# Optimization experiments

Measured on AMD Instinct MI355X. Metric: run time of the kernel, lower is better.

Reference implementation:

```python
import jax, jax.numpy as jnp
import numpy as np

NG = 100000   # num gene nodes
ND = 100000   # num disease nodes
E = 400000    # edges per edge type
EL = 200000   # label edges
C = 128       # hidden_channels


def segment_softmax(logits, seg, n):
    # PyG-style softmax over segments (numerically stable, eps=1e-16)
    m = jax.ops.segment_max(logits, seg, num_segments=n)
    e = jnp.exp(logits - m[seg])
    s = jax.ops.segment_sum(e, seg, num_segments=n)
    return e / (s[seg] + 1e-16)


def hgat_edge_type(x_src, x_dst, src_idx, dst_idx, edge_emb, wi, wj, we, att_b, n_dst):
    # gather (message), per-edge attention logit = [x_i|x_j|e] @ w  (split to avoid concat)
    x_i = x_dst[dst_idx]                                   # [E, C]
    x_j = x_src[src_idx]                                   # [E, C]
    logit = x_i @ wi + x_j @ wj + edge_emb @ we + att_b    # [E, 1] (num_heads=1)
    alpha = jax.nn.leaky_relu(logit, 0.2)
    alpha = segment_softmax(alpha, dst_idx, n_dst)
    out = jax.ops.segment_sum(x_i * alpha, dst_idx, num_segments=n_dst)  # scatter-add
    return jax.nn.relu(out)


def setup_inputs() -> dict:
    key = jax.random.key(0)
    ks = jax.random.split(key, 24)
    s = 0.02
    return {
        "x_gene": jax.random.normal(ks[0], (NG, C), jnp.float32),
        "x_disease": jax.random.normal(ks[1], (ND, C), jnp.float32),
        "edge_index_g2d": jnp.stack([jax.random.randint(ks[2], (E,), 0, NG),
                                     jax.random.randint(ks[3], (E,), 0, ND)]),
        "edge_index_d2g": jnp.stack([jax.random.randint(ks[4], (E,), 0, ND),
                                     jax.random.randint(ks[5], (E,), 0, NG)]),
        "edge_emb_g2d": jax.random.normal(ks[6], (E, C), jnp.float32),
        "edge_emb_d2g": jax.random.normal(ks[7], (E, C), jnp.float32),
        "edge_label_index": jnp.stack([jax.random.randint(ks[8], (EL,), 0, NG),
                                       jax.random.randint(ks[9], (EL,), 0, ND)]),
        # HeteroDictLinear node / edge weights (stored [in, out])
        "Wn_gene": jax.random.normal(ks[10], (C, C), jnp.float32) * s,
        "bn_gene": jnp.zeros((C,), jnp.float32),
        "Wn_disease": jax.random.normal(ks[11], (C, C), jnp.float32) * s,
        "bn_disease": jnp.zeros((C,), jnp.float32),
        "We_g2d": jax.random.normal(ks[12], (C, C), jnp.float32) * s,
        "be_g2d": jnp.zeros((C,), jnp.float32),
        "We_d2g": jax.random.normal(ks[13], (C, C), jnp.float32) * s,
        "be_d2g": jnp.zeros((C,), jnp.float32),
        # attention head: Linear(3*C, 1) applied to cat([x_i, x_j, edge_emb])
        "att_w": jax.random.normal(ks[14], (3 * C, 1), jnp.float32) * s,
        "att_b": jnp.zeros((1,), jnp.float32),
        # decoder
        "W1": jax.random.normal(ks[15], (2 * C, C), jnp.float32) * s,
        "b1": jnp.zeros((C,), jnp.float32),
        "W2": jax.random.normal(ks[16], (C, 1), jnp.float32) * s,
        "b2": jnp.zeros((1,), jnp.float32),
    }


def reference(x_gene, x_disease, edge_index_g2d, edge_index_d2g, edge_emb_g2d,
              edge_emb_d2g, edge_label_index, Wn_gene, bn_gene, Wn_disease,
              bn_disease, We_g2d, be_g2d, We_d2g, be_d2g, att_w, att_b,
              W1, b1, W2, b2):
    # per-type node / edge linear projections
    x_g = x_gene @ Wn_gene + bn_gene
    x_d = x_disease @ Wn_disease + bn_disease
    e_g2d = edge_emb_g2d @ We_g2d + be_g2d
    e_d2g = edge_emb_d2g @ We_d2g + be_d2g
    wi, wj, we = att_w[:C], att_w[C:2 * C], att_w[2 * C:]
    # gene->disease aggregates into disease nodes; disease->gene into gene nodes
    z_disease = hgat_edge_type(x_g, x_d, edge_index_g2d[0], edge_index_g2d[1],
                               e_g2d, wi, wj, we, att_b, ND)
    z_gene = hgat_edge_type(x_d, x_g, edge_index_d2g[0], edge_index_d2g[1],
                            e_d2g, wi, wj, we, att_b, NG)
    # decoder on label edges
    row, col = edge_label_index[0], edge_label_index[1]
    z = jnp.concatenate([z_gene[row], z_disease[col]], axis=-1)  # [EL, 2C]
    h = jax.nn.relu(z @ W1 + b1)
    pred = (h @ W2 + b2).reshape(-1)                             # [EL]
    return pred, z_gene, z_disease
```

## Files before the change

### kernel.cpp

```cpp
#include <hip/hip_runtime.h>
#include <hip/hip_bf16.h>
#include <stdint.h>

#define NGn 100000
#define NDn 100000
#define NEn 400000
#define ELn 200000

typedef __bf16 bf16x8 __attribute__((ext_vector_type(8)));
typedef float  f32x4  __attribute__((ext_vector_type(4)));

__device__ __forceinline__ bf16x8 cvt8(const float* __restrict__ f) {
    f32x4 a = *(const f32x4*)f;
    f32x4 b = *(const f32x4*)(f + 4);
    bf16x8 r;
    r[0] = (__bf16)a[0]; r[1] = (__bf16)a[1]; r[2] = (__bf16)a[2]; r[3] = (__bf16)a[3];
    r[4] = (__bf16)b[0]; r[5] = (__bf16)b[1]; r[6] = (__bf16)b[2]; r[7] = (__bf16)b[3];
    return r;
}

__global__ void scatter_mask(const int* __restrict__ g2d_dst,
                             const int* __restrict__ d2g_dst,
                             uint8_t* __restrict__ mask_d,
                             uint8_t* __restrict__ mask_g, int n) {
    int i = blockIdx.x * blockDim.x + threadIdx.x;
    if (i < n) {
        mask_d[g2d_dst[i]] = 1;
        mask_g[d2g_dst[i]] = 1;
    }
}

__global__ __launch_bounds__(256) void node_gemm(
    const float* __restrict__ X, const float* __restrict__ W,
    const float* __restrict__ bias, const uint8_t* __restrict__ mask,
    float* __restrict__ Zf, __bf16* __restrict__ Zb, int Nrows)
{
    __shared__ __bf16 Wt[128 * 136];
    const int tid = threadIdx.x;
    for (int idx = tid; idx < 128 * 128; idx += 256) {
        int k = idx >> 7, c = idx & 127;
        Wt[c * 136 + k] = (__bf16)W[idx];
    }
    __syncthreads();

    const int wave = tid >> 6;
    const int lane = tid & 63;
    const int m = lane & 15;
    const int q = lane >> 4;

    float bcol[8];
#pragma unroll
    for (int nt = 0; nt < 8; ++nt) bcol[nt] = bias[nt * 16 + m];

    const int ntiles = (Nrows + 63) >> 6;
    for (int t = blockIdx.x; t < ntiles; t += gridDim.x) {
        const int base = t * 64;
        const int row_a = base + wave * 16 + m;
        const int rowa_c = row_a < Nrows ? row_a : (Nrows - 1);

        f32x4 acc[8];
#pragma unroll
        for (int nt = 0; nt < 8; ++nt) acc[nt] = f32x4{0.f, 0.f, 0.f, 0.f};

#pragma unroll
        for (int kk = 0; kk < 4; ++kk) {
            bf16x8 a = cvt8(X + (size_t)rowa_c * 128 + kk * 32 + q * 8);
#pragma unroll
            for (int nt = 0; nt < 8; ++nt) {
                bf16x8 b = *(const bf16x8*)(&Wt[(nt * 16 + m) * 136 + kk * 32 + q * 8]);
                acc[nt] = __builtin_amdgcn_mfma_f32_16x16x32_bf16(a, b, acc[nt], 0, 0, 0);
            }
        }

#pragma unroll
        for (int reg = 0; reg < 4; ++reg) {
            int r = base + wave * 16 + q * 4 + reg;
            if (r < Nrows) {
                float mk = mask[r] ? 1.f : 0.f;
#pragma unroll
                for (int nt = 0; nt < 8; ++nt) {
                    float v = acc[nt][reg] + bcol[nt];
                    v = (v > 0.f ? v : 0.f) * mk;
                    Zf[(size_t)r * 128 + nt * 16 + m] = v;
                    if (Zb) Zb[(size_t)r * 128 + nt * 16 + m] = (__bf16)v;
                }
            }
        }
    }
}

__global__ __launch_bounds__(256) void mlp_kernel(
    const __bf16* __restrict__ zgb, const __bf16* __restrict__ zdb,
    const float* __restrict__ zgf, const float* __restrict__ zdf,
    int usebf, const int* __restrict__ eli,
    const float* __restrict__ W1, const float* __restrict__ b1,
    const float* __restrict__ W2, const float* __restrict__ b2,
    float* __restrict__ pred)
{
    __shared__ __bf16 Wt[128 * 256];
    const int tid = threadIdx.x;
    for (int idx = tid; idx < 256 * 128; idx += 256) {
        int k = idx >> 7, c = idx & 127;
        int kc = k >> 3, kl = k & 7;
        Wt[c * 256 + ((kc ^ (c & 7)) * 8 + kl)] = (__bf16)W1[idx];
    }
    __syncthreads();

    const int wave = tid >> 6;
    const int lane = tid & 63;
    const int m = lane & 15;
    const int q = lane >> 4;

    float b1c[8], w2c[8];
#pragma unroll
    for (int nt = 0; nt < 8; ++nt) {
        b1c[nt] = b1[nt * 16 + m];
        w2c[nt] = W2[nt * 16 + m];
    }
    const float bb = b2[0];

    const int ngroups = ELn / 64;
    for (int g = blockIdx.x; g < ngroups; g += gridDim.x) {
        const int e = g * 64 + wave * 16 + m;
        const int grow = eli[e];
        const int dcol = eli[ELn + e];

        f32x4 acc[8];
#pragma unroll
        for (int nt = 0; nt < 8; ++nt) acc[nt] = f32x4{0.f, 0.f, 0.f, 0.f};

#pragma unroll
        for (int kk = 0; kk < 8; ++kk) {
            bf16x8 a;
            if (usebf) {
                const __bf16* src = (kk < 4) ? (zgb + (size_t)grow * 128 + kk * 32)
                                             : (zdb + (size_t)dcol * 128 + (kk - 4) * 32);
                a = *(const bf16x8*)(src + q * 8);
            } else {
                const float* src = (kk < 4) ? (zgf + (size_t)grow * 128 + kk * 32)
                                            : (zdf + (size_t)dcol * 128 + (kk - 4) * 32);
                a = cvt8(src + q * 8);
            }
            const int kcr = kk * 4 + q;
#pragma unroll
            for (int nt = 0; nt < 8; ++nt) {
                int n = nt * 16 + m;
                bf16x8 b = *(const bf16x8*)(&Wt[n * 256 + ((kcr ^ (n & 7)) * 8)]);
                acc[nt] = __builtin_amdgcn_mfma_f32_16x16x32_bf16(a, b, acc[nt], 0, 0, 0);
            }
        }

        float pb[4];
#pragma unroll
        for (int reg = 0; reg < 4; ++reg) {
            float s = 0.f;
#pragma unroll
            for (int nt = 0; nt < 8; ++nt) {
                float h = acc[nt][reg] + b1c[nt];
                h = h > 0.f ? h : 0.f;
                s += h * w2c[nt];
            }
            pb[reg] = s;
        }
#pragma unroll
        for (int off = 1; off < 16; off <<= 1) {
#pragma unroll
            for (int reg = 0; reg < 4; ++reg)
                pb[reg] += __shfl_xor(pb[reg], off, 64);
        }
        if (m == 0) {
#pragma unroll
            for (int reg = 0; reg < 4; ++reg) {
                int er = g * 64 + wave * 16 + q * 4 + reg;
                pred[er] = pb[reg] + bb;
            }
        }
    }
}

extern "C" void kernel_launch(void* const* d_in, const int* in_sizes, int n_in,
                              void* d_out, int out_size, void* d_ws, size_t ws_size,
                              hipStream_t stream) {
    const float* x_gene    = (const float*)d_in[0];
    const float* x_disease = (const float*)d_in[1];
    const int*   ei_g2d    = (const int*)d_in[2];
    const int*   ei_d2g    = (const int*)d_in[3];
    const int*   eli       = (const int*)d_in[6];
    const float* Wn_gene   = (const float*)d_in[7];
    const float* bn_gene   = (const float*)d_in[8];
    const float* Wn_dis    = (const float*)d_in[9];
    const float* bn_dis    = (const float*)d_in[10];
    const float* W1        = (const float*)d_in[17];
    const float* b1        = (const float*)d_in[18];
    const float* W2        = (const float*)d_in[19];
    const float* b2        = (const float*)d_in[20];

    float* out   = (float*)d_out;
    float* predp = out;
    float* zgf   = out + ELn;
    float* zdf   = zgf + (size_t)NGn * 128;

    uint8_t* mask_d = (uint8_t*)d_ws;
    uint8_t* mask_g = mask_d + NDn;

    const size_t zelems = (size_t)NGn * 128;
    const size_t mirror_off = 200704;
    const bool   mirror = ws_size >= mirror_off + 2 * zelems * sizeof(__bf16);
    __bf16* zgb = mirror ? (__bf16*)((char*)d_ws + mirror_off) : nullptr;
    __bf16* zdb = mirror ? zgb + zelems : nullptr;

    hipMemsetAsync(d_ws, 0, NGn + NDn, stream);
    scatter_mask<<<(NEn + 255) / 256, 256, 0, stream>>>(
        ei_g2d + NEn, ei_d2g + NEn, mask_d, mask_g, NEn);

    node_gemm<<<1024, 256, 0, stream>>>(x_gene, Wn_gene, bn_gene, mask_g, zgf, zgb, NGn);
    node_gemm<<<1024, 256, 0, stream>>>(x_disease, Wn_dis, bn_dis, mask_d, zdf, zdb, NDn);

    mlp_kernel<<<512, 256, 0, stream>>>(zgb, zdb, zgf, zdf, mirror ? 1 : 0,
                                        eli, W1, b1, W2, b2, predp);
}
```

Measured before the change: 533.6 us.

## Precompute per-node W1 projections and reduce label-edge MLP to gather-add

Splits the decoder's first linear layer algebraically: each node's z is multiplied by its half of W1 once per node (100k+100k rows), instead of once per label edge (200k edges with 256-wide inputs). The edge kernel then only gathers two projected bf16 rows, adds bias, applies ReLU and does the W2 dot product with a shuffle reduction. This needs extra workspace for two more bf16 node buffers and an extra pass writing them, and it falls back to the old kernel when the workspace is too small.

```diff
diff --git a/kernel.cpp b/kernel.cpp
--- a/kernel.cpp
+++ b/kernel.cpp
@@ -85,6 +85,118 @@
                     if (Zb) Zb[(size_t)r * 128 + nt * 16 + m] = (__bf16)v;
                 }
             }
+        }
+    }
+}
+
+__global__ __launch_bounds__(256) void h_gemm(
+    const __bf16* __restrict__ Zgb, const __bf16* __restrict__ Zdb,
+    const float* __restrict__ W1,
+    __bf16* __restrict__ Hgb, __bf16* __restrict__ Hdb)
+{
+    __shared__ __bf16 Wt[128 * 136];
+    const int half = gridDim.x >> 1;
+    const bool gene = (int)blockIdx.x < half;
+    const __bf16* __restrict__ Z = gene ? Zgb : Zdb;
+    __bf16*       __restrict__ H = gene ? Hgb : Hdb;
+    const float*  __restrict__ Ws = W1 + (gene ? 0 : 128 * 128);
+
+    const int tid = threadIdx.x;
+    for (int idx = tid; idx < 128 * 128; idx += 256) {
+        int k = idx >> 7, c = idx & 127;
+        Wt[c * 136 + k] = (__bf16)Ws[idx];
+    }
+    __syncthreads();
+
+    const int wave = tid >> 6;
+    const int lane = tid & 63;
+    const int m = lane & 15;
+    const int q = lane >> 4;
+
+    const int ntiles = (NGn + 63) >> 6;
+    const int b0 = gene ? (int)blockIdx.x : (int)blockIdx.x - half;
+    for (int t = b0; t < ntiles; t += half) {
+        const int base = t * 64;
+        const int row_a = base + wave * 16 + m;
+        const int rowa_c = row_a < NGn ? row_a : (NGn - 1);
+
+        f32x4 acc[8];
+#pragma unroll
+        for (int nt = 0; nt < 8; ++nt) acc[nt] = f32x4{0.f, 0.f, 0.f, 0.f};
+
+#pragma unroll
+        for (int kk = 0; kk < 4; ++kk) {
+            bf16x8 a = *(const bf16x8*)(Z + (size_t)rowa_c * 128 + kk * 32 + q * 8);
+#pragma unroll
+            for (int nt = 0; nt < 8; ++nt) {
+                bf16x8 b = *(const bf16x8*)(&Wt[(nt * 16 + m) * 136 + kk * 32 + q * 8]);
+                acc[nt] = __builtin_amdgcn_mfma_f32_16x16x32_bf16(a, b, acc[nt], 0, 0, 0);
+            }
+        }
+
+#pragma unroll
+        for (int reg = 0; reg < 4; ++reg) {
+            int r = base + wave * 16 + q * 4 + reg;
+            if (r < NGn) {
+#pragma unroll
+                for (int nt = 0; nt < 8; ++nt)
+                    H[(size_t)r * 128 + nt * 16 + m] = (__bf16)acc[nt][reg];
+            }
+        }
+    }
+}
+
+__global__ __launch_bounds__(256) void edge_mlp(
+    const __bf16* __restrict__ Hgb, const __bf16* __restrict__ Hdb,
+    const int* __restrict__ eli, const float* __restrict__ b1,
+    const float* __restrict__ W2, const float* __restrict__ b2,
+    float* __restrict__ pred)
+{
+    const int tid = threadIdx.x;
+    const int wave = tid >> 6;
+    const int lane = tid & 63;
+    const int l16 = lane & 15;
+    const int sub = lane >> 4;
+
+    float b1c[8], w2c[8];
+#pragma unroll
+    for (int j = 0; j < 8; ++j) {
+        b1c[j] = b1[l16 * 8 + j];
+        w2c[j] = W2[l16 * 8 + j];
+    }
+    const float bb = b2[0];
+
+    const int nunits = ELn >> 3;
+    const int wid0 = (int)blockIdx.x * 4 + wave;
+    const int wstride = (int)gridDim.x * 4;
+    for (int u = wid0; u < nunits; u += wstride) {
+        const int e0 = u * 8 + sub * 2;
+        const int g0 = eli[e0],       g1 = eli[e0 + 1];
+        const int d0 = eli[ELn + e0], d1 = eli[ELn + e0 + 1];
+
+        bf16x8 vg0 = *(const bf16x8*)(Hgb + (size_t)g0 * 128 + l16 * 8);
+        bf16x8 vd0 = *(const bf16x8*)(Hdb + (size_t)d0 * 128 + l16 * 8);
+        bf16x8 vg1 = *(const bf16x8*)(Hgb + (size_t)g1 * 128 + l16 * 8);
+        bf16x8 vd1 = *(const bf16x8*)(Hdb + (size_t)d1 * 128 + l16 * 8);
+
+        float s0 = 0.f, s1 = 0.f;
+#pragma unroll
+        for (int j = 0; j < 8; ++j) {
+            float h0 = (float)vg0[j] + (float)vd0[j] + b1c[j];
+            float h1 = (float)vg1[j] + (float)vd1[j] + b1c[j];
+            h0 = h0 > 0.f ? h0 : 0.f;
+            h1 = h1 > 0.f ? h1 : 0.f;
+            s0 += h0 * w2c[j];
+            s1 += h1 * w2c[j];
+        }
+#pragma unroll
+        for (int off = 1; off < 16; off <<= 1) {
+            s0 += __shfl_xor(s0, off, 64);
+            s1 += __shfl_xor(s1, off, 64);
+        }
+        if (l16 == 0) {
+            pred[e0]     = s0 + bb;
+            pred[e0 + 1] = s1 + bb;
         }
     }
 }
@@ -205,9 +317,12 @@
 
     const size_t zelems = (size_t)NGn * 128;
     const size_t mirror_off = 200704;
-    const bool   mirror = ws_size >= mirror_off + 2 * zelems * sizeof(__bf16);
-    __bf16* zgb = mirror ? (__bf16*)((char*)d_ws + mirror_off) : nullptr;
-    __bf16* zdb = mirror ? zgb + zelems : nullptr;
+    const bool   mirror2 = ws_size >= mirror_off + 2 * zelems * sizeof(__bf16);
+    const bool   mirror4 = ws_size >= mirror_off + 4 * zelems * sizeof(__bf16);
+    __bf16* zgb = mirror2 ? (__bf16*)((char*)d_ws + mirror_off) : nullptr;
+    __bf16* zdb = mirror2 ? zgb + zelems : nullptr;
+    __bf16* Hgb = mirror4 ? zdb + zelems : nullptr;
+    __bf16* Hdb = mirror4 ? Hgb + zelems : nullptr;
 
     hipMemsetAsync(d_ws, 0, NGn + NDn, stream);
     scatter_mask<<<(NEn + 255) / 256, 256, 0, stream>>>(
@@ -216,6 +331,11 @@
     node_gemm<<<1024, 256, 0, stream>>>(x_gene, Wn_gene, bn_gene, mask_g, zgf, zgb, NGn);
     node_gemm<<<1024, 256, 0, stream>>>(x_disease, Wn_dis, bn_dis, mask_d, zdf, zdb, NDn);
 
-    mlp_kernel<<<512, 256, 0, stream>>>(zgb, zdb, zgf, zdf, mirror ? 1 : 0,
-                                        eli, W1, b1, W2, b2, predp);
-}
+    if (mirror4) {
+        h_gemm<<<2048, 256, 0, stream>>>(zgb, zdb, W1, Hgb, Hdb);
+        edge_mlp<<<2048, 256, 0, stream>>>(Hgb, Hdb, eli, b1, W2, b2, predp);
+    } else {
+        mlp_kernel<<<512, 256, 0, stream>>>(zgb, zdb, zgf, zdf, mirror2 ? 1 : 0,
+                                            eli, W1, b1, W2, b2, predp);
+    }
+}
```

Result: no change. 525.0 us (-1.6%).
